# Optimization experiments

Hardware: AMD Instinct MI355X
Metric: run time of the kernel (lower is better)

The kernel has to match this reference:

```python
import jax, jax.numpy as jnp
import numpy as np
import math

HIDDEN = 512
N_PROTO = 1024
BATCH = 16384


def setup_inputs() -> dict:
    key = jax.random.key(0)
    kx, kp = jax.random.split(key)
    X = jax.random.normal(kx, (BATCH, HIDDEN), dtype=jnp.float32)
    # prototypes init: uniform in [-k, k], k = 1/sqrt(hidden)
    k = 1.0 / math.sqrt(HIDDEN)
    u = jax.random.uniform(kp, (N_PROTO, HIDDEN), dtype=jnp.float32)
    prototypes = k + (-2.0 * k) * u
    return {"X": X, "prototypes": prototypes}


def reference(X, prototypes):
    # out[b, p] = -sum_h (X[b,h] - prototypes[p,h])^2
    x_sq = jnp.sum(X * X, axis=1, keepdims=True)            # [B, 1]
    p_sq = jnp.sum(prototypes * prototypes, axis=1)[None, :]  # [1, P]
    cross = jnp.einsum("bh,ph->bp", X, prototypes)          # [B, P]
    return -(x_sq + p_sq - 2.0 * cross)
```

## Files before the change

kernel.cpp:

```cpp
#include <hip/hip_runtime.h>
#include <hip/hip_bf16.h>

#define MDIM 16384
#define NDIM 1024
#define KDIM 512
#define BM 128
#define BN 128
#define BK 64

typedef __attribute__((ext_vector_type(8))) short bf16x8;
typedef __attribute__((ext_vector_type(4))) float f32x4;

__device__ __forceinline__ short f2bf(float f) {
    union { float f; unsigned u; } v; v.f = f;
    unsigned r = v.u + 0x7fff + ((v.u >> 16) & 1);
    return (short)(r >> 16);
}

__device__ __forceinline__ bf16x8 cvt8(float4 a, float4 b) {
    bf16x8 o;
    o[0] = f2bf(a.x); o[1] = f2bf(a.y); o[2] = f2bf(a.z); o[3] = f2bf(a.w);
    o[4] = f2bf(b.x); o[5] = f2bf(b.y); o[6] = f2bf(b.z); o[7] = f2bf(b.w);
    return o;
}

__device__ __forceinline__ void gload_lds16(const void* g, void* l) {
    __builtin_amdgcn_global_load_lds(
        (const __attribute__((address_space(1))) void*)g,
        (__attribute__((address_space(3))) void*)l, 16, 0, 0);
}

__global__ __launch_bounds__(256) void convert_sumsq(
        const float* __restrict__ X, const float* __restrict__ P,
        short* __restrict__ Xbf, short* __restrict__ Pbf,
        float* __restrict__ xsq, float* __restrict__ psq) {
    int wave = (blockIdx.x * blockDim.x + threadIdx.x) >> 6;
    int lane = threadIdx.x & 63;
    const float* src; short* dstb; float* dsts; int row;
    if (wave < MDIM) { src = X; dstb = Xbf; dsts = xsq; row = wave; }
    else             { src = P; dstb = Pbf; dsts = psq; row = wave - MDIM; }
    const float4* r4 = (const float4*)(src + (size_t)row * KDIM) + lane * 2;
    float4 a = r4[0], b = r4[1];
    *(bf16x8*)(dstb + (size_t)row * KDIM + lane * 8) = cvt8(a, b);
    float s = a.x*a.x + a.y*a.y + a.z*a.z + a.w*a.w
            + b.x*b.x + b.y*b.y + b.z*b.z + b.w*b.w;
    #pragma unroll
    for (int off = 32; off; off >>= 1) s += __shfl_down(s, off, 64);
    if (lane == 0) dsts[row] = s;
}

__global__ __launch_bounds__(256) void dist_gemm_bf(
        const short* __restrict__ Xbf, const short* __restrict__ Pbf,
        const float* __restrict__ xsq, const float* __restrict__ psq,
        float* __restrict__ out) {
    __shared__ short As[BM * BK];
    __shared__ short Bs[BN * BK];

    int tid = threadIdx.x;
    int bid = blockIdx.x;
    int swz = (bid & 7) * 128 + (bid >> 3);
    int bn = swz & 7, bm = swz >> 3;
    int row0 = bm * BM, col0 = bn * BN;

    int lane = tid & 63, wid = tid >> 6;
    int wm = (wid >> 1) * 64, wn = (wid & 1) * 64;

    f32x4 acc[4][4] = {};

    const short* Ab = Xbf + (size_t)row0 * KDIM;
    const short* Bb = Pbf + (size_t)col0 * KDIM;

    for (int kt = 0; kt < KDIM / BK; ++kt) {
        __syncthreads();
        #pragma unroll
        for (int i = 0; i < 4; ++i) {
            int c = tid + 256 * i;
            int row = c >> 3;
            int g16 = (c & 7) ^ (row & 7);
            const char* ga = (const char*)(Ab + (size_t)row * KDIM)
                             + kt * (BK * 2) + g16 * 16;
            const char* gb = (const char*)(Bb + (size_t)row * KDIM)
                             + kt * (BK * 2) + g16 * 16;
            char* la = (char*)As + i * 4096 + wid * 1024;
            char* lb = (char*)Bs + i * 4096 + wid * 1024;
            gload_lds16(ga, la);
            gload_lds16(gb, lb);
        }
        __syncthreads();
        #pragma unroll
        for (int ks = 0; ks < 2; ++ks) {
            bf16x8 af[4], bfr[4];
            int kb = ks * 64 + ((lane >> 4) * 16);
            #pragma unroll
            for (int m = 0; m < 4; ++m) {
                int row = wm + m * 16 + (lane & 15);
                int off = (row * (BK * 2) + kb) ^ ((row & 7) << 4);
                af[m] = *(const bf16x8*)((const char*)As + off);
            }
            #pragma unroll
            for (int n = 0; n < 4; ++n) {
                int row = wn + n * 16 + (lane & 15);
                int off = (row * (BK * 2) + kb) ^ ((row & 7) << 4);
                bfr[n] = *(const bf16x8*)((const char*)Bs + off);
            }
            #pragma unroll
            for (int m = 0; m < 4; ++m)
                #pragma unroll
                for (int n = 0; n < 4; ++n)
                    acc[m][n] = __builtin_amdgcn_mfma_f32_16x16x32_bf16(
                        af[m], bfr[n], acc[m][n], 0, 0, 0);
        }
    }

    int cr = (lane >> 4) * 4;
    int cc = lane & 15;
    #pragma unroll
    for (int n = 0; n < 4; ++n) {
        int gc = col0 + wn + n * 16 + cc;
        float ps = psq[gc];
        #pragma unroll
        for (int m = 0; m < 4; ++m) {
            int grb = row0 + wm + m * 16 + cr;
            #pragma unroll
            for (int r = 0; r < 4; ++r) {
                float v = 2.0f * acc[m][n][r] - xsq[grb + r] - ps;
                out[(size_t)(grb + r) * NDIM + gc] = v;
            }
        }
    }
}

__global__ __launch_bounds__(256) void sumsq_kernel(
        const float* __restrict__ X, const float* __restrict__ P,
        float* __restrict__ xsq, float* __restrict__ psq) {
    int wave = (blockIdx.x * blockDim.x + threadIdx.x) >> 6;
    int lane = threadIdx.x & 63;
    const float* src; float* dst; int row;
    if (wave < MDIM) { src = X; dst = xsq; row = wave; }
    else             { src = P; dst = psq; row = wave - MDIM; }
    const float4* r4 = (const float4*)(src + (size_t)row * KDIM) + lane * 2;
    float4 a = r4[0], b = r4[1];
    float s = a.x*a.x + a.y*a.y + a.z*a.z + a.w*a.w
            + b.x*b.x + b.y*b.y + b.z*b.z + b.w*b.w;
    #pragma unroll
    for (int off = 32; off; off >>= 1) s += __shfl_down(s, off, 64);
    if (lane == 0) dst[row] = s;
}

__global__ __launch_bounds__(256) void dist_gemm(
        const float* __restrict__ X, const float* __restrict__ P,
        const float* __restrict__ xsq, const float* __restrict__ psq,
        float* __restrict__ out) {
    __shared__ short As[BM * BK];
    __shared__ short Bs[BN * BK];
    int tid = threadIdx.x;
    int bid = blockIdx.x;
    int swz = (bid & 7) * 128 + (bid >> 3);
    int bn = swz & 7, bm = swz >> 3;
    int row0 = bm * BM, col0 = bn * BN;
    int lane = tid & 63, wid = tid >> 6;
    int wm = (wid >> 1) * 64, wn = (wid & 1) * 64;
    f32x4 acc[4][4] = {};
    int rbase = tid >> 3;
    int kg = tid & 7;
    const float* Abase = X + (size_t)row0 * KDIM;
    const float* Bbase = P + (size_t)col0 * KDIM;
    for (int kt = 0; kt < KDIM / BK; ++kt) {
        int kofs = kt * BK + kg * 8;
        __syncthreads();
        #pragma unroll
        for (int i = 0; i < 4; ++i) {
            int row = rbase + 32 * i;
            const float4* ga = (const float4*)(Abase + (size_t)row * KDIM + kofs);
            float4 a0 = ga[0], a1 = ga[1];
            const float4* gb = (const float4*)(Bbase + (size_t)row * KDIM + kofs);
            float4 b0 = gb[0], b1 = gb[1];
            int off = (row * (BK * 2) + kg * 16) ^ ((row & 7) << 4);
            *(bf16x8*)((char*)As + off) = cvt8(a0, a1);
            *(bf16x8*)((char*)Bs + off) = cvt8(b0, b1);
        }
        __syncthreads();
        #pragma unroll
        for (int ks = 0; ks < 2; ++ks) {
            bf16x8 af[4], bfr[4];
            int kb = ks * 64 + ((lane >> 4) * 16);
            #pragma unroll
            for (int m = 0; m < 4; ++m) {
                int row = wm + m * 16 + (lane & 15);
                int off = (row * (BK * 2) + kb) ^ ((row & 7) << 4);
                af[m] = *(const bf16x8*)((const char*)As + off);
            }
            #pragma unroll
            for (int n = 0; n < 4; ++n) {
                int row = wn + n * 16 + (lane & 15);
                int off = (row * (BK * 2) + kb) ^ ((row & 7) << 4);
                bfr[n] = *(const bf16x8*)((const char*)Bs + off);
            }
            #pragma unroll
            for (int m = 0; m < 4; ++m)
                #pragma unroll
                for (int n = 0; n < 4; ++n)
                    acc[m][n] = __builtin_amdgcn_mfma_f32_16x16x32_bf16(
                        af[m], bfr[n], acc[m][n], 0, 0, 0);
        }
    }
    int cr = (lane >> 4) * 4;
    int cc = lane & 15;
    #pragma unroll
    for (int n = 0; n < 4; ++n) {
        int gc = col0 + wn + n * 16 + cc;
        float ps = psq[gc];
        #pragma unroll
        for (int m = 0; m < 4; ++m) {
            int grb = row0 + wm + m * 16 + cr;
            #pragma unroll
            for (int r = 0; r < 4; ++r) {
                float v = 2.0f * acc[m][n][r] - xsq[grb + r] - ps;
                out[(size_t)(grb + r) * NDIM + gc] = v;
            }
        }
    }
}

extern "C" void kernel_launch(void* const* d_in, const int* in_sizes, int n_in,
                              void* d_out, int out_size, void* d_ws, size_t ws_size,
                              hipStream_t stream) {
    const float* X = (const float*)d_in[0];
    const float* P = (const float*)d_in[1];
    float* out = (float*)d_out;

    const size_t bf_elems = (size_t)(MDIM + NDIM) * KDIM;
    const size_t need = bf_elems * 2 + (size_t)(MDIM + NDIM) * 4;

    if (ws_size >= need) {
        short* Xbf = (short*)d_ws;
        short* Pbf = Xbf + (size_t)MDIM * KDIM;
        float* xsq = (float*)(Xbf + bf_elems);
        float* psq = xsq + MDIM;
        convert_sumsq<<<(MDIM + NDIM) / 4, 256, 0, stream>>>(X, P, Xbf, Pbf, xsq, psq);
        dist_gemm_bf<<<(MDIM / BM) * (NDIM / BN), 256, 0, stream>>>(Xbf, Pbf, xsq, psq, out);
    } else {
        float* xsq = (float*)d_ws;
        float* psq = xsq + MDIM;
        sumsq_kernel<<<(MDIM + NDIM) / 4, 256, 0, stream>>>(X, P, xsq, psq);
        dist_gemm<<<(MDIM / BM) * (NDIM / BN), 256, 0, stream>>>(X, P, xsq, psq, out);
    }
}
```

Before: 44.89 us.

## Use 256x256 tiles with 512 threads and double-buffered LDS in bf16 GEMM

```diff
diff --git a/kernel.cpp b/kernel.cpp
--- a/kernel.cpp
+++ b/kernel.cpp
@@ -4,9 +4,10 @@
 #define MDIM 16384
 #define NDIM 1024
 #define KDIM 512
-#define BM 128
-#define BN 128
+#define BM 256
+#define BN 256
 #define BK 64
+#define KTILES (KDIM / BK)
 
 typedef __attribute__((ext_vector_type(8))) short bf16x8;
 typedef __attribute__((ext_vector_type(4))) float f32x4;
@@ -49,82 +50,95 @@
     if (lane == 0) dsts[row] = s;
 }
 
-__global__ __launch_bounds__(256) void dist_gemm_bf(
+__global__ __launch_bounds__(512, 2) void dist_gemm_bf2(
         const short* __restrict__ Xbf, const short* __restrict__ Pbf,
         const float* __restrict__ xsq, const float* __restrict__ psq,
         float* __restrict__ out) {
-    __shared__ short As[BM * BK];
-    __shared__ short Bs[BN * BK];
+    __shared__ short As[2][BM * BK];
+    __shared__ short Bs[2][BN * BK];
 
     int tid = threadIdx.x;
     int bid = blockIdx.x;
-    int swz = (bid & 7) * 128 + (bid >> 3);
-    int bn = swz & 7, bm = swz >> 3;
+    int swz = (bid & 7) * 32 + (bid >> 3);
+    int bn = swz & 3, bm = swz >> 2;
     int row0 = bm * BM, col0 = bn * BN;
 
     int lane = tid & 63, wid = tid >> 6;
-    int wm = (wid >> 1) * 64, wn = (wid & 1) * 64;
-
-    f32x4 acc[4][4] = {};
+    int wr = wid >> 2, wc = wid & 3;
+
+    f32x4 acc[8][4] = {};
 
     const short* Ab = Xbf + (size_t)row0 * KDIM;
     const short* Bb = Pbf + (size_t)col0 * KDIM;
 
-    for (int kt = 0; kt < KDIM / BK; ++kt) {
-        __syncthreads();
+    auto stage = [&](int sel, int kt) {
         #pragma unroll
         for (int i = 0; i < 4; ++i) {
-            int c = tid + 256 * i;
+            int c = tid + 512 * i;
             int row = c >> 3;
             int g16 = (c & 7) ^ (row & 7);
             const char* ga = (const char*)(Ab + (size_t)row * KDIM)
                              + kt * (BK * 2) + g16 * 16;
             const char* gb = (const char*)(Bb + (size_t)row * KDIM)
                              + kt * (BK * 2) + g16 * 16;
-            char* la = (char*)As + i * 4096 + wid * 1024;
-            char* lb = (char*)Bs + i * 4096 + wid * 1024;
+            char* la = (char*)&As[sel][0] + i * 8192 + wid * 1024;
+            char* lb = (char*)&Bs[sel][0] + i * 8192 + wid * 1024;
             gload_lds16(ga, la);
             gload_lds16(gb, lb);
         }
-        __syncthreads();
+    };
+
+    auto compute = [&](int sel) {
         #pragma unroll
         for (int ks = 0; ks < 2; ++ks) {
-            bf16x8 af[4], bfr[4];
             int kb = ks * 64 + ((lane >> 4) * 16);
-            #pragma unroll
-            for (int m = 0; m < 4; ++m) {
-                int row = wm + m * 16 + (lane & 15);
-                int off = (row * (BK * 2) + kb) ^ ((row & 7) << 4);
-                af[m] = *(const bf16x8*)((const char*)As + off);
-            }
+            bf16x8 bfr[4];
             #pragma unroll
             for (int n = 0; n < 4; ++n) {
-                int row = wn + n * 16 + (lane & 15);
-                int off = (row * (BK * 2) + kb) ^ ((row & 7) << 4);
-                bfr[n] = *(const bf16x8*)((const char*)Bs + off);
-            }
-            #pragma unroll
-            for (int m = 0; m < 4; ++m)
+                int row = wc * 64 + n * 16 + (lane & 15);
+                int off = (row * (BK * 2) + kb) ^ ((row & 7) << 4);
+                bfr[n] = *(const bf16x8*)((const char*)&Bs[sel][0] + off);
+            }
+            #pragma unroll
+            for (int m = 0; m < 8; ++m) {
+                int row = wr * 128 + m * 16 + (lane & 15);
+                int off = (row * (BK * 2) + kb) ^ ((row & 7) << 4);
+                bf16x8 af = *(const bf16x8*)((const char*)&As[sel][0] + off);
                 #pragma unroll
                 for (int n = 0; n < 4; ++n)
                     acc[m][n] = __builtin_amdgcn_mfma_f32_16x16x32_bf16(
-                        af[m], bfr[n], acc[m][n], 0, 0, 0);
-        }
-    }
+                        af, bfr[n], acc[m][n], 0, 0, 0);
+            }
+        }
+    };
+
+    stage(0, 0);
+    __syncthreads();
+    int cur = 0;
+    for (int kt = 0; kt < KTILES - 1; ++kt) {
+        stage(cur ^ 1, kt + 1);
+        compute(cur);
+        __syncthreads();
+        cur ^= 1;
+    }
+    compute(cur);
 
     int cr = (lane >> 4) * 4;
     int cc = lane & 15;
-    #pragma unroll
-    for (int n = 0; n < 4; ++n) {
-        int gc = col0 + wn + n * 16 + cc;
-        float ps = psq[gc];
-        #pragma unroll
-        for (int m = 0; m < 4; ++m) {
-            int grb = row0 + wm + m * 16 + cr;
-            #pragma unroll
-            for (int r = 0; r < 4; ++r) {
-                float v = 2.0f * acc[m][n][r] - xsq[grb + r] - ps;
-                out[(size_t)(grb + r) * NDIM + gc] = v;
+    float ps[4];
+    #pragma unroll
+    for (int n = 0; n < 4; ++n) ps[n] = psq[col0 + wc * 64 + n * 16 + cc];
+    #pragma unroll
+    for (int m = 0; m < 8; ++m) {
+        int grb = row0 + wr * 128 + m * 16 + cr;
+        #pragma unroll
+        for (int r = 0; r < 4; ++r) {
+            float xv = xsq[grb + r];
+            size_t ob = (size_t)(grb + r) * NDIM;
+            #pragma unroll
+            for (int n = 0; n < 4; ++n) {
+                int gc = col0 + wc * 64 + n * 16 + cc;
+                out[ob + gc] = 2.0f * acc[m][n][r] - xv - ps[n];
             }
         }
     }
@@ -151,13 +165,13 @@
         const float* __restrict__ X, const float* __restrict__ P,
         const float* __restrict__ xsq, const float* __restrict__ psq,
         float* __restrict__ out) {
-    __shared__ short As[BM * BK];
-    __shared__ short Bs[BN * BK];
+    __shared__ short As[128 * BK];
+    __shared__ short Bs[128 * BK];
     int tid = threadIdx.x;
     int bid = blockIdx.x;
     int swz = (bid & 7) * 128 + (bid >> 3);
     int bn = swz & 7, bm = swz >> 3;
-    int row0 = bm * BM, col0 = bn * BN;
+    int row0 = bm * 128, col0 = bn * 128;
     int lane = tid & 63, wid = tid >> 6;
     int wm = (wid >> 1) * 64, wn = (wid & 1) * 64;
     f32x4 acc[4][4] = {};
@@ -238,11 +252,11 @@
         float* xsq = (float*)(Xbf + bf_elems);
         float* psq = xsq + MDIM;
         convert_sumsq<<<(MDIM + NDIM) / 4, 256, 0, stream>>>(X, P, Xbf, Pbf, xsq, psq);
-        dist_gemm_bf<<<(MDIM / BM) * (NDIM / BN), 256, 0, stream>>>(Xbf, Pbf, xsq, psq, out);
+        dist_gemm_bf2<<<(MDIM / BM) * (NDIM / BN), 512, 0, stream>>>(Xbf, Pbf, xsq, psq, out);
     } else {
         float* xsq = (float*)d_ws;
         float* psq = xsq + MDIM;
         sumsq_kernel<<<(MDIM + NDIM) / 4, 256, 0, stream>>>(X, P, xsq, psq);
-        dist_gemm<<<(MDIM / BM) * (NDIM / BN), 256, 0, stream>>>(X, P, xsq, psq, out);
-    }
-}
+        dist_gemm<<<(MDIM / 128) * (NDIM / 128), 256, 0, stream>>>(X, P, xsq, psq, out);
+    }
+}
```

Measured after the change: 40.02 us. 1.12x faster.

## Fuse X conversion into GEMM with row-block-resident LDS tile and double-buffered B

Applied to the files above, without the earlier changes.

```diff
diff --git a/kernel.cpp b/kernel.cpp
--- a/kernel.cpp
+++ b/kernel.cpp
@@ -4,11 +4,14 @@
 #define MDIM 16384
 #define NDIM 1024
 #define KDIM 512
-#define BM 128
-#define BN 128
+#define ROWS 64
+#define BN 256
 #define BK 64
+#define NBN (NDIM / BN)
+#define KT (KDIM / BK)
 
 typedef __attribute__((ext_vector_type(8))) short bf16x8;
+typedef __attribute__((ext_vector_type(4))) short bf16x4;
 typedef __attribute__((ext_vector_type(4))) float f32x4;
 
 __device__ __forceinline__ short f2bf(float f) {
@@ -17,115 +20,136 @@
     return (short)(r >> 16);
 }
 
-__device__ __forceinline__ bf16x8 cvt8(float4 a, float4 b) {
-    bf16x8 o;
-    o[0] = f2bf(a.x); o[1] = f2bf(a.y); o[2] = f2bf(a.z); o[3] = f2bf(a.w);
-    o[4] = f2bf(b.x); o[5] = f2bf(b.y); o[6] = f2bf(b.z); o[7] = f2bf(b.w);
-    return o;
-}
-
 __device__ __forceinline__ void gload_lds16(const void* g, void* l) {
     __builtin_amdgcn_global_load_lds(
         (const __attribute__((address_space(1))) void*)g,
         (__attribute__((address_space(3))) void*)l, 16, 0, 0);
 }
 
-__global__ __launch_bounds__(256) void convert_sumsq(
-        const float* __restrict__ X, const float* __restrict__ P,
-        short* __restrict__ Xbf, short* __restrict__ Pbf,
-        float* __restrict__ xsq, float* __restrict__ psq) {
+__global__ __launch_bounds__(256) void convert_p(
+        const float* __restrict__ P, short* __restrict__ Pbf,
+        float* __restrict__ psq) {
     int wave = (blockIdx.x * blockDim.x + threadIdx.x) >> 6;
     int lane = threadIdx.x & 63;
-    const float* src; short* dstb; float* dsts; int row;
-    if (wave < MDIM) { src = X; dstb = Xbf; dsts = xsq; row = wave; }
-    else             { src = P; dstb = Pbf; dsts = psq; row = wave - MDIM; }
-    const float4* r4 = (const float4*)(src + (size_t)row * KDIM) + lane * 2;
+    const float4* r4 = (const float4*)(P + (size_t)wave * KDIM) + lane * 2;
     float4 a = r4[0], b = r4[1];
-    *(bf16x8*)(dstb + (size_t)row * KDIM + lane * 8) = cvt8(a, b);
+    bf16x8 o;
+    o[0] = f2bf(a.x); o[1] = f2bf(a.y); o[2] = f2bf(a.z); o[3] = f2bf(a.w);
+    o[4] = f2bf(b.x); o[5] = f2bf(b.y); o[6] = f2bf(b.z); o[7] = f2bf(b.w);
+    *(bf16x8*)(Pbf + (size_t)wave * KDIM + lane * 8) = o;
     float s = a.x*a.x + a.y*a.y + a.z*a.z + a.w*a.w
             + b.x*b.x + b.y*b.y + b.z*b.z + b.w*b.w;
     #pragma unroll
     for (int off = 32; off; off >>= 1) s += __shfl_down(s, off, 64);
-    if (lane == 0) dsts[row] = s;
-}
-
-__global__ __launch_bounds__(256) void dist_gemm_bf(
-        const short* __restrict__ Xbf, const short* __restrict__ Pbf,
-        const float* __restrict__ xsq, const float* __restrict__ psq,
-        float* __restrict__ out) {
-    __shared__ short As[BM * BK];
-    __shared__ short Bs[BN * BK];
+    if (lane == 0) psq[wave] = s;
+}
+
+__global__ __launch_bounds__(256, 1) void dist_persist(
+        const float* __restrict__ X, const short* __restrict__ Pbf,
+        const float* __restrict__ psq, float* __restrict__ out) {
+    __shared__ short Al[ROWS * KDIM];
+    __shared__ short Bsl[2][BN * BK];
+    __shared__ float xs_l[ROWS];
 
     int tid = threadIdx.x;
     int bid = blockIdx.x;
-    int swz = (bid & 7) * 128 + (bid >> 3);
-    int bn = swz & 7, bm = swz >> 3;
-    int row0 = bm * BM, col0 = bn * BN;
+    int row0 = bid * ROWS;
 
     int lane = tid & 63, wid = tid >> 6;
-    int wm = (wid >> 1) * 64, wn = (wid & 1) * 64;
-
-    f32x4 acc[4][4] = {};
-
-    const short* Ab = Xbf + (size_t)row0 * KDIM;
-    const short* Bb = Pbf + (size_t)col0 * KDIM;
-
-    for (int kt = 0; kt < KDIM / BK; ++kt) {
-        __syncthreads();
-        #pragma unroll
-        for (int i = 0; i < 4; ++i) {
-            int c = tid + 256 * i;
+    int wc = wid;
+
+    auto stageB = [&](int sel, int bnb, int kt) {
+        #pragma unroll
+        for (int s = 0; s < 8; ++s) {
+            int c = s * 256 + tid;
             int row = c >> 3;
             int g16 = (c & 7) ^ (row & 7);
-            const char* ga = (const char*)(Ab + (size_t)row * KDIM)
+            const char* gb = (const char*)(Pbf + (size_t)(bnb * BN + row) * KDIM)
                              + kt * (BK * 2) + g16 * 16;
-            const char* gb = (const char*)(Bb + (size_t)row * KDIM)
-                             + kt * (BK * 2) + g16 * 16;
-            char* la = (char*)As + i * 4096 + wid * 1024;
-            char* lb = (char*)Bs + i * 4096 + wid * 1024;
-            gload_lds16(ga, la);
-            gload_lds16(gb, lb);
-        }
-        __syncthreads();
-        #pragma unroll
-        for (int ks = 0; ks < 2; ++ks) {
-            bf16x8 af[4], bfr[4];
-            int kb = ks * 64 + ((lane >> 4) * 16);
-            #pragma unroll
-            for (int m = 0; m < 4; ++m) {
-                int row = wm + m * 16 + (lane & 15);
-                int off = (row * (BK * 2) + kb) ^ ((row & 7) << 4);
-                af[m] = *(const bf16x8*)((const char*)As + off);
-            }
-            #pragma unroll
-            for (int n = 0; n < 4; ++n) {
-                int row = wn + n * 16 + (lane & 15);
-                int off = (row * (BK * 2) + kb) ^ ((row & 7) << 4);
-                bfr[n] = *(const bf16x8*)((const char*)Bs + off);
-            }
-            #pragma unroll
-            for (int m = 0; m < 4; ++m)
-                #pragma unroll
-                for (int n = 0; n < 4; ++n)
-                    acc[m][n] = __builtin_amdgcn_mfma_f32_16x16x32_bf16(
-                        af[m], bfr[n], acc[m][n], 0, 0, 0);
-        }
-    }
+            gload_lds16(gb, (char*)&Bsl[sel][0] + s * 4096 + wid * 1024);
+        }
+    };
+
+    stageB(0, 0, 0);
+
+    {
+        int arow = tid >> 2, q = tid & 3;
+        const float4* rp = (const float4*)(X + (size_t)(row0 + arow) * KDIM);
+        float ssq = 0.f;
+        #pragma unroll
+        for (int i = 0; i < 32; ++i) {
+            int col4 = i * 4 + q;
+            float4 a = rp[col4];
+            ssq += a.x * a.x + a.y * a.y + a.z * a.z + a.w * a.w;
+            bf16x4 av;
+            av[0] = f2bf(a.x); av[1] = f2bf(a.y); av[2] = f2bf(a.z); av[3] = f2bf(a.w);
+            int off = (arow * (KDIM * 2) + col4 * 8) ^ ((arow & 7) << 4);
+            *(bf16x4*)((char*)Al + off) = av;
+        }
+        ssq += __shfl_xor(ssq, 1, 64);
+        ssq += __shfl_xor(ssq, 2, 64);
+        if (q == 0) xs_l[arow] = ssq;
+    }
+    __syncthreads();
 
     int cr = (lane >> 4) * 4;
     int cc = lane & 15;
-    #pragma unroll
-    for (int n = 0; n < 4; ++n) {
-        int gc = col0 + wn + n * 16 + cc;
-        float ps = psq[gc];
-        #pragma unroll
-        for (int m = 0; m < 4; ++m) {
-            int grb = row0 + wm + m * 16 + cr;
-            #pragma unroll
-            for (int r = 0; r < 4; ++r) {
-                float v = 2.0f * acc[m][n][r] - xsq[grb + r] - ps;
-                out[(size_t)(grb + r) * NDIM + gc] = v;
-            }
+
+    #pragma unroll 1
+    for (int bn = 0; bn < NBN; ++bn) {
+        f32x4 acc[4][4] = {};
+        #pragma unroll
+        for (int kt = 0; kt < KT; ++kt) {
+            int buf = kt & 1;
+            if (kt < KT - 1)            stageB(buf ^ 1, bn, kt + 1);
+            else if (bn < NBN - 1)      stageB(buf ^ 1, bn + 1, 0);
+            const char* aB = (const char*)Al;
+            const char* bB = (const char*)&Bsl[buf][0];
+            #pragma unroll
+            for (int ks = 0; ks < 2; ++ks) {
+                int kbB = ks * 64 + ((lane >> 4) * 16);
+                int kbA = kt * 128 + kbB;
+                bf16x8 af[4], bfr[4];
+                #pragma unroll
+                for (int m = 0; m < 4; ++m) {
+                    int row = m * 16 + (lane & 15);
+                    af[m] = *(const bf16x8*)(aB +
+                        ((row * (KDIM * 2) + kbA) ^ ((row & 7) << 4)));
+                }
+                #pragma unroll
+                for (int n = 0; n < 4; ++n) {
+                    int row = wc * 64 + n * 16 + (lane & 15);
+                    bfr[n] = *(const bf16x8*)(bB +
+                        ((row * (BK * 2) + kbB) ^ ((row & 7) << 4)));
+                }
+                #pragma unroll
+                for (int m = 0; m < 4; ++m)
+                    #pragma unroll
+                    for (int n = 0; n < 4; ++n)
+                        acc[m][n] = __builtin_amdgcn_mfma_f32_16x16x32_bf16(
+                            af[m], bfr[n], acc[m][n], 0, 0, 0);
+            }
+            if (kt == KT - 1) {
+                float ps[4];
+                #pragma unroll
+                for (int n = 0; n < 4; ++n)
+                    ps[n] = psq[bn * BN + wc * 64 + n * 16 + cc];
+                #pragma unroll
+                for (int m = 0; m < 4; ++m) {
+                    #pragma unroll
+                    for (int r = 0; r < 4; ++r) {
+                        int lr = m * 16 + cr + r;
+                        float xv = xs_l[lr];
+                        size_t ob = (size_t)(row0 + lr) * NDIM + bn * BN;
+                        #pragma unroll
+                        for (int n = 0; n < 4; ++n)
+                            out[ob + wc * 64 + n * 16 + cc] =
+                                2.0f * acc[m][n][r] - xv - ps[n];
+                    }
+                }
+            }
+            if (!(bn == NBN - 1 && kt == KT - 1))
+                __syncthreads();
         }
     }
 }
@@ -147,17 +171,24 @@
     if (lane == 0) dst[row] = s;
 }
 
+__device__ __forceinline__ bf16x8 cvt8(float4 a, float4 b) {
+    bf16x8 o;
+    o[0] = f2bf(a.x); o[1] = f2bf(a.y); o[2] = f2bf(a.z); o[3] = f2bf(a.w);
+    o[4] = f2bf(b.x); o[5] = f2bf(b.y); o[6] = f2bf(b.z); o[7] = f2bf(b.w);
+    return o;
+}
+
 __global__ __launch_bounds__(256) void dist_gemm(
         const float* __restrict__ X, const float* __restrict__ P,
         const float* __restrict__ xsq, const float* __restrict__ psq,
         float* __restrict__ out) {
-    __shared__ short As[BM * BK];
-    __shared__ short Bs[BN * BK];
+    __shared__ short As[128 * BK];
+    __shared__ short Bs[128 * BK];
     int tid = threadIdx.x;
     int bid = blockIdx.x;
     int swz = (bid & 7) * 128 + (bid >> 3);
     int bn = swz & 7, bm = swz >> 3;
-    int row0 = bm * BM, col0 = bn * BN;
+    int row0 = bm * 128, col0 = bn * 128;
     int lane = tid & 63, wid = tid >> 6;
     int wm = (wid >> 1) * 64, wn = (wid & 1) * 64;
     f32x4 acc[4][4] = {};
@@ -229,20 +260,17 @@
     const float* P = (const float*)d_in[1];
     float* out = (float*)d_out;
 
-    const size_t bf_elems = (size_t)(MDIM + NDIM) * KDIM;
-    const size_t need = bf_elems * 2 + (size_t)(MDIM + NDIM) * 4;
+    const size_t need = (size_t)NDIM * KDIM * 2 + (size_t)NDIM * 4;
 
     if (ws_size >= need) {
-        short* Xbf = (short*)d_ws;
-        short* Pbf = Xbf + (size_t)MDIM * KDIM;
-        float* xsq = (float*)(Xbf + bf_elems);
-        float* psq = xsq + MDIM;
-        convert_sumsq<<<(MDIM + NDIM) / 4, 256, 0, stream>>>(X, P, Xbf, Pbf, xsq, psq);
-        dist_gemm_bf<<<(MDIM / BM) * (NDIM / BN), 256, 0, stream>>>(Xbf, Pbf, xsq, psq, out);
+        short* Pbf = (short*)d_ws;
+        float* psq = (float*)(Pbf + (size_t)NDIM * KDIM);
+        convert_p<<<NDIM / 4, 256, 0, stream>>>(P, Pbf, psq);
+        dist_persist<<<MDIM / ROWS, 256, 0, stream>>>(X, Pbf, psq, out);
     } else {
         float* xsq = (float*)d_ws;
         float* psq = xsq + MDIM;
         sumsq_kernel<<<(MDIM + NDIM) / 4, 256, 0, stream>>>(X, P, xsq, psq);
-        dist_gemm<<<(MDIM / BM) * (NDIM / BN), 256, 0, stream>>>(X, P, xsq, psq, out);
-    }
-}
+        dist_gemm<<<(MDIM / 128) * (NDIM / 128), 256, 0, stream>>>(X, P, xsq, psq, out);
+    }
+}
```

New measurement: 51.52 us. 1.15x slower.

## Stream A fragments from global and keep a full-K prototype tile in LDS

Applied to the files above, without the earlier changes.

```diff
diff --git a/kernel.cpp b/kernel.cpp
--- a/kernel.cpp
+++ b/kernel.cpp
@@ -4,9 +4,9 @@
 #define MDIM 16384
 #define NDIM 1024
 #define KDIM 512
-#define BM 128
-#define BN 128
-#define BK 64
+#define BCOL 128
+#define BROW 512
+#define NKS (KDIM / 32)
 
 typedef __attribute__((ext_vector_type(8))) short bf16x8;
 typedef __attribute__((ext_vector_type(4))) float f32x4;
@@ -49,83 +49,75 @@
     if (lane == 0) dsts[row] = s;
 }
 
-__global__ __launch_bounds__(256) void dist_gemm_bf(
+__global__ __launch_bounds__(512, 2) void dist_stream(
         const short* __restrict__ Xbf, const short* __restrict__ Pbf,
         const float* __restrict__ xsq, const float* __restrict__ psq,
         float* __restrict__ out) {
-    __shared__ short As[BM * BK];
-    __shared__ short Bs[BN * BK];
+    __shared__ short Bl[BCOL * KDIM];
 
     int tid = threadIdx.x;
     int bid = blockIdx.x;
-    int swz = (bid & 7) * 128 + (bid >> 3);
-    int bn = swz & 7, bm = swz >> 3;
-    int row0 = bm * BM, col0 = bn * BN;
+    int xcd = bid & 7, i = bid >> 3;
+    int rowg = xcd * 4 + (i & 3);
+    int colg = i >> 2;
+    int row0 = rowg * BROW, col0 = colg * BCOL;
 
     int lane = tid & 63, wid = tid >> 6;
-    int wm = (wid >> 1) * 64, wn = (wid & 1) * 64;
-
-    f32x4 acc[4][4] = {};
-
-    const short* Ab = Xbf + (size_t)row0 * KDIM;
-    const short* Bb = Pbf + (size_t)col0 * KDIM;
-
-    for (int kt = 0; kt < KDIM / BK; ++kt) {
-        __syncthreads();
-        #pragma unroll
-        for (int i = 0; i < 4; ++i) {
-            int c = tid + 256 * i;
-            int row = c >> 3;
-            int g16 = (c & 7) ^ (row & 7);
-            const char* ga = (const char*)(Ab + (size_t)row * KDIM)
-                             + kt * (BK * 2) + g16 * 16;
-            const char* gb = (const char*)(Bb + (size_t)row * KDIM)
-                             + kt * (BK * 2) + g16 * 16;
-            char* la = (char*)As + i * 4096 + wid * 1024;
-            char* lb = (char*)Bs + i * 4096 + wid * 1024;
-            gload_lds16(ga, la);
-            gload_lds16(gb, lb);
-        }
-        __syncthreads();
-        #pragma unroll
-        for (int ks = 0; ks < 2; ++ks) {
-            bf16x8 af[4], bfr[4];
-            int kb = ks * 64 + ((lane >> 4) * 16);
-            #pragma unroll
-            for (int m = 0; m < 4; ++m) {
-                int row = wm + m * 16 + (lane & 15);
-                int off = (row * (BK * 2) + kb) ^ ((row & 7) << 4);
-                af[m] = *(const bf16x8*)((const char*)As + off);
-            }
-            #pragma unroll
-            for (int n = 0; n < 4; ++n) {
-                int row = wn + n * 16 + (lane & 15);
-                int off = (row * (BK * 2) + kb) ^ ((row & 7) << 4);
-                bfr[n] = *(const bf16x8*)((const char*)Bs + off);
-            }
-            #pragma unroll
-            for (int m = 0; m < 4; ++m)
-                #pragma unroll
-                for (int n = 0; n < 4; ++n)
-                    acc[m][n] = __builtin_amdgcn_mfma_f32_16x16x32_bf16(
-                        af[m], bfr[n], acc[m][n], 0, 0, 0);
-        }
+
+    #pragma unroll
+    for (int s = 0; s < 16; ++s) {
+        int col = s * 8 + wid;
+        int slot2 = (lane & 56) | ((lane & 7) ^ (col & 7));
+        const char* g = (const char*)(Pbf + (size_t)(col0 + col) * KDIM)
+                        + slot2 * 16;
+        gload_lds16(g, (char*)Bl + col * 1024);
+    }
+    __syncthreads();
+
+    int wrow0 = row0 + wid * 64;
+    const char* arow[4];
+    #pragma unroll
+    for (int m = 0; m < 4; ++m)
+        arow[m] = (const char*)(Xbf + (size_t)(wrow0 + m * 16 + (lane & 15)) * KDIM);
+    int kg16 = (lane >> 4) * 16;
+
+    f32x4 acc[4][8] = {};
+    #pragma unroll
+    for (int ks = 0; ks < NKS; ++ks) {
+        int kb = ks * 64 + kg16;
+        bf16x8 af[4], bfr[8];
+        #pragma unroll
+        for (int m = 0; m < 4; ++m)
+            af[m] = *(const bf16x8*)(arow[m] + kb);
+        #pragma unroll
+        for (int n = 0; n < 8; ++n) {
+            int col = n * 16 + (lane & 15);
+            bfr[n] = *(const bf16x8*)((const char*)Bl +
+                        ((col * 1024 + kb) ^ ((col & 7) << 4)));
+        }
+        #pragma unroll
+        for (int m = 0; m < 4; ++m)
+            #pragma unroll
+            for (int n = 0; n < 8; ++n)
+                acc[m][n] = __builtin_amdgcn_mfma_f32_16x16x32_bf16(
+                    af[m], bfr[n], acc[m][n], 0, 0, 0);
     }
 
     int cr = (lane >> 4) * 4;
     int cc = lane & 15;
-    #pragma unroll
-    for (int n = 0; n < 4; ++n) {
-        int gc = col0 + wn + n * 16 + cc;
-        float ps = psq[gc];
-        #pragma unroll
-        for (int m = 0; m < 4; ++m) {
-            int grb = row0 + wm + m * 16 + cr;
-            #pragma unroll
-            for (int r = 0; r < 4; ++r) {
-                float v = 2.0f * acc[m][n][r] - xsq[grb + r] - ps;
-                out[(size_t)(grb + r) * NDIM + gc] = v;
-            }
+    float ps[8];
+    #pragma unroll
+    for (int n = 0; n < 8; ++n) ps[n] = psq[col0 + n * 16 + cc];
+    #pragma unroll
+    for (int m = 0; m < 4; ++m) {
+        #pragma unroll
+        for (int r = 0; r < 4; ++r) {
+            int row = wrow0 + m * 16 + cr + r;
+            float xv = xsq[row];
+            size_t ob = (size_t)row * NDIM + col0;
+            #pragma unroll
+            for (int n = 0; n < 8; ++n)
+                out[ob + n * 16 + cc] = 2.0f * acc[m][n][r] - xv - ps[n];
         }
     }
 }
@@ -151,13 +143,13 @@
         const float* __restrict__ X, const float* __restrict__ P,
         const float* __restrict__ xsq, const float* __restrict__ psq,
         float* __restrict__ out) {
-    __shared__ short As[BM * BK];
-    __shared__ short Bs[BN * BK];
+    __shared__ short As[128 * 64];
+    __shared__ short Bs[128 * 64];
     int tid = threadIdx.x;
     int bid = blockIdx.x;
     int swz = (bid & 7) * 128 + (bid >> 3);
     int bn = swz & 7, bm = swz >> 3;
-    int row0 = bm * BM, col0 = bn * BN;
+    int row0 = bm * 128, col0 = bn * 128;
     int lane = tid & 63, wid = tid >> 6;
     int wm = (wid >> 1) * 64, wn = (wid & 1) * 64;
     f32x4 acc[4][4] = {};
@@ -165,8 +157,8 @@
     int kg = tid & 7;
     const float* Abase = X + (size_t)row0 * KDIM;
     const float* Bbase = P + (size_t)col0 * KDIM;
-    for (int kt = 0; kt < KDIM / BK; ++kt) {
-        int kofs = kt * BK + kg * 8;
+    for (int kt = 0; kt < KDIM / 64; ++kt) {
+        int kofs = kt * 64 + kg * 8;
         __syncthreads();
         #pragma unroll
         for (int i = 0; i < 4; ++i) {
@@ -175,7 +167,7 @@
             float4 a0 = ga[0], a1 = ga[1];
             const float4* gb = (const float4*)(Bbase + (size_t)row * KDIM + kofs);
             float4 b0 = gb[0], b1 = gb[1];
-            int off = (row * (BK * 2) + kg * 16) ^ ((row & 7) << 4);
+            int off = (row * 128 + kg * 16) ^ ((row & 7) << 4);
             *(bf16x8*)((char*)As + off) = cvt8(a0, a1);
             *(bf16x8*)((char*)Bs + off) = cvt8(b0, b1);
         }
@@ -187,13 +179,13 @@
             #pragma unroll
             for (int m = 0; m < 4; ++m) {
                 int row = wm + m * 16 + (lane & 15);
-                int off = (row * (BK * 2) + kb) ^ ((row & 7) << 4);
+                int off = (row * 128 + kb) ^ ((row & 7) << 4);
                 af[m] = *(const bf16x8*)((const char*)As + off);
             }
             #pragma unroll
             for (int n = 0; n < 4; ++n) {
                 int row = wn + n * 16 + (lane & 15);
-                int off = (row * (BK * 2) + kb) ^ ((row & 7) << 4);
+                int off = (row * 128 + kb) ^ ((row & 7) << 4);
                 bfr[n] = *(const bf16x8*)((const char*)Bs + off);
             }
             #pragma unroll
@@ -238,11 +230,11 @@
         float* xsq = (float*)(Xbf + bf_elems);
         float* psq = xsq + MDIM;
         convert_sumsq<<<(MDIM + NDIM) / 4, 256, 0, stream>>>(X, P, Xbf, Pbf, xsq, psq);
-        dist_gemm_bf<<<(MDIM / BM) * (NDIM / BN), 256, 0, stream>>>(Xbf, Pbf, xsq, psq, out);
+        dist_stream<<<(MDIM / BROW) * (NDIM / BCOL), 512, 0, stream>>>(Xbf, Pbf, xsq, psq, out);
     } else {
         float* xsq = (float*)d_ws;
         float* psq = xsq + MDIM;
         sumsq_kernel<<<(MDIM + NDIM) / 4, 256, 0, stream>>>(X, P, xsq, psq);
-        dist_gemm<<<(MDIM / BM) * (NDIM / BN), 256, 0, stream>>>(X, P, xsq, psq, out);
-    }
-}
+        dist_gemm<<<(MDIM / 128) * (NDIM / 128), 256, 0, stream>>>(X, P, xsq, psq, out);
+    }
+}
```

Measured after the change: 42.76 us. -4.8%, faster.
